# Performance work log

Hardware: AMD Instinct MI355X
Metric: run time of the kernel (lower is better)

Reference implementation:

```python
import jax, jax.numpy as jnp
import numpy as np

H = 64  # lstm hidden

def _lstm_scan(xs, h0, c0, wih, whh, bih, bhh):
    # xs: [T,B,D]; torch gate order i,f,g,o
    def step(carry, xt):
        h, c = carry
        gates = xt @ wih.T + h @ whh.T + bih + bhh
        i, f, g, o = jnp.split(gates, 4, axis=-1)
        c = jax.nn.sigmoid(f) * c + jax.nn.sigmoid(i) * jnp.tanh(g)
        h = jax.nn.sigmoid(o) * jnp.tanh(c)
        return (h, c), h
    (h, c), hs = jax.lax.scan(step, (h0, c0), xs)
    return hs, h, c


def setup_inputs() -> dict:
    key = jax.random.key(0)
    ks = jax.random.split(key, 32)
    r = lambda i, shape: (jax.random.normal(ks[i], shape, jnp.float32) * 0.05)
    B, T = 2048, 128
    inp = {
        "x": jax.random.normal(ks[0], (B, T, 37), jnp.float32),
        "enc_lin_w": r(1, (64, 37)), "enc_lin_b": r(2, (64,)),
        "enc_wih_f": r(3, (4 * H, 64)), "enc_whh_f": r(4, (4 * H, H)),
        "enc_bih_f": r(5, (4 * H,)), "enc_bhh_f": r(6, (4 * H,)),
        "enc_wih_b": r(7, (4 * H, 64)), "enc_whh_b": r(8, (4 * H, H)),
        "enc_bih_b": r(9, (4 * H,)), "enc_bhh_b": r(10, (4 * H,)),
        "att1_w": r(11, (32, 192)), "att1_b": r(12, (32,)),
        "att2_w": r(13, (1, 32)), "att2_b": r(14, (1,)),
        "dec_wih": r(15, (4 * H, 128)), "dec_whh": r(16, (4 * H, H)),
        "dec_bih": r(17, (4 * H,)), "dec_bhh": r(18, (4 * H,)),
        "dec_lin_w": r(19, (11, H)), "dec_lin_b": r(20, (11,)),
        "output_len": 10,
    }
    return inp


def reference(x, enc_lin_w, enc_lin_b,
              enc_wih_f, enc_whh_f, enc_bih_f, enc_bhh_f,
              enc_wih_b, enc_whh_b, enc_bih_b, enc_bhh_b,
              att1_w, att1_b, att2_w, att2_b,
              dec_wih, dec_whh, dec_bih, dec_bhh,
              dec_lin_w, dec_lin_b, output_len):
    B, T, _ = x.shape
    # ---- Encoder: linear -> relu -> BiLSTM ----
    e = jax.nn.relu(x @ enc_lin_w.T + enc_lin_b)          # [B,T,64]
    xs = jnp.transpose(e, (1, 0, 2))                       # [T,B,64]
    z = jnp.zeros((B, H), x.dtype)
    hf, _, _ = _lstm_scan(xs, z, z, enc_wih_f, enc_whh_f, enc_bih_f, enc_bhh_f)
    hb, _, _ = _lstm_scan(xs[::-1], z, z, enc_wih_b, enc_whh_b, enc_bih_b, enc_bhh_b)
    feats = jnp.concatenate([hf, hb[::-1]], axis=-1)       # [T,B,128]
    feats = jnp.transpose(feats, (1, 0, 2))                # [B,T,128]

    # ---- Decoder loop with (degenerate) additive attention ----
    def dec_step(carry, _):
        h, c = carry
        h_rep = jnp.broadcast_to(h[:, None, :], (B, T, H))
        fin = jnp.concatenate([feats, h_rep], axis=-1)     # [B,T,192]
        a = jnp.tanh(fin @ att1_w.T + att1_b)              # [B,T,32]
        s = a @ att2_w.T + att2_b                          # [B,T,1]
        scores = jax.nn.softmax(s, axis=-1)                # all ones (faithful to source)
        fd = jnp.sum(feats * scores, axis=1)               # [B,128]
        gates = fd @ dec_wih.T + h @ dec_whh.T + dec_bih + dec_bhh
        i, f, g, o = jnp.split(gates, 4, axis=-1)
        c = jax.nn.sigmoid(f) * c + jax.nn.sigmoid(i) * jnp.tanh(g)
        h = jax.nn.sigmoid(o) * jnp.tanh(c)
        out = jax.nn.softmax(h @ dec_lin_w.T + dec_lin_b, axis=-1)  # [B,11]
        return (h, c), out

    (_, _), outs = jax.lax.scan(dec_step, (z, z), None, length=output_len)
    return jnp.transpose(outs, (1, 0, 2))                  # [B,output_len,11]
```

## Files before the change

kernel.cpp:

```cpp
#include <hip/hip_runtime.h>


typedef _Float16 f16;
typedef f16 f16x8 __attribute__((ext_vector_type(8)));
typedef float f32x4 __attribute__((ext_vector_type(4)));

#define MFMA16(a, b, c) __builtin_amdgcn_mfma_f32_16x16x32_f16(a, b, c, 0, 0, 0)

__device__ __forceinline__ float sigf(float x) { return 1.f / (1.f + __expf(-x)); }
__device__ __forceinline__ float tanhf_fast(float x) {
  float e = __expf(2.f * x);
  return 1.f - 2.f / (e + 1.f);
}

#define NLOG2E  -1.4426950408889634f
#define N2LOG2E -2.8853900817779268f

__device__ __forceinline__ float rcp_(float x) { return __builtin_amdgcn_rcpf(x); }
__device__ __forceinline__ float ex2_(float x) { return __builtin_amdgcn_exp2f(x); }


__global__ __launch_bounds__(256) void enc_linear_k(
    const float* __restrict__ x, const float* __restrict__ w1,
    const float* __restrict__ b1, f16* __restrict__ efrag) {
  const int t = blockIdx.y;
  const int bblock = blockIdx.x;
  const int tid = threadIdx.x;
  const int w = tid >> 6, l = tid & 63;
  const int rho = l & 15, c = l >> 4;

  __shared__ float ldsw[64 * 37];
  __shared__ float ldsb[64];
  __shared__ __align__(16) f16 ldse[4][2][64][8];

  for (int i = tid; i < 64 * 37; i += 256) ldsw[i] = w1[i];
  if (tid < 64) ldsb[tid] = b1[tid];
  __syncthreads();

  f16x8 bw[4][2];
#pragma unroll
  for (int nt = 0; nt < 4; nt++) {
    const int kout = nt * 16 + rho;
#pragma unroll
    for (int ks = 0; ks < 2; ks++) {
      f16x8 v;
#pragma unroll
      for (int i = 0; i < 8; i++) {
        const int d = ks * 32 + c * 8 + i;
        v[i] = (f16)(d < 37 ? ldsw[kout * 37 + d] : 0.f);
      }
      bw[nt][ks] = v;
    }
  }

  const int brow = bblock * 64 + w * 16 + rho;
  const float* xrow = x + ((size_t)brow * 128 + t) * 37;
  f16x8 a0, a1;
#pragma unroll
  for (int i = 0; i < 8; i++) a0[i] = (f16)xrow[c * 8 + i];
#pragma unroll
  for (int i = 0; i < 8; i++) {
    const int d = 32 + c * 8 + i;
    a1[i] = (f16)((c == 0 && d < 37) ? xrow[d] : 0.f);
  }

  f32x4 acc[4] = {};
#pragma unroll
  for (int nt = 0; nt < 4; nt++) {
    acc[nt] = MFMA16(a0, bw[nt][0], acc[nt]);
    acc[nt] = MFMA16(a1, bw[nt][1], acc[nt]);
  }

#pragma unroll
  for (int nt = 0; nt < 4; nt++) {
    const int k = nt * 16 + rho;
#pragma unroll
    for (int r = 0; r < 4; r++) {
      const int bi = c * 4 + r;
      float v = acc[nt][r] + ldsb[k];
      v = fmaxf(v, 0.f);
      ldse[w][k >> 5][bi | (((k >> 3) & 3) << 4)][k & 7] = (f16)v;
    }
  }
  __syncthreads();
  const int bg = bblock * 4 + w;
  float4* dst = (float4*)efrag + ((size_t)(t * 128 + bg) * 2) * 64;
  const float4* src = (const float4*)&ldse[w][0][0][0];
  dst[l] = src[l];
  dst[64 + l] = src[64 + l];
}

__global__ __launch_bounds__(512, 2) void bilstm_k(
    const f16* __restrict__ efrag,
    const float* __restrict__ wih_f, const float* __restrict__ whh_f,
    const float* __restrict__ bih_f, const float* __restrict__ bhh_f,
    const float* __restrict__ wih_b, const float* __restrict__ whh_b,
    const float* __restrict__ bih_b, const float* __restrict__ bhh_b,
    float* __restrict__ fd) {
  const int bid = blockIdx.x;
  const int dir = bid >> 7;
  const int bg = bid & 127;
  const int tid = threadIdx.x;
  const int w = tid >> 6, l = tid & 63;
  const int rho = l & 15, c = l >> 4;
  const int gate = rho & 3, uoff = rho >> 2;

  const float* wih = dir ? wih_b : wih_f;
  const float* whh = dir ? whh_b : whh_f;
  const float* bih = dir ? bih_b : bih_f;
  const float* bhh = dir ? bhh_b : bhh_f;

  __shared__ __align__(16) f16 hbuf[2][2][64][8];
  {
    int* hz = (int*)hbuf;
    for (int i = tid; i < (int)(sizeof(hbuf) / 4); i += 512) hz[i] = 0;
  }

  const float sA = (gate == 2) ? N2LOG2E : NLOG2E;

  f16x8 aih[2][2], ahh[2][2];
#pragma unroll
  for (int q = 0; q < 2; q++) {
    const int m = 2 * w + q;
    const int n = gate * 64 + 4 * m + uoff;
#pragma unroll
    for (int ks = 0; ks < 2; ks++) {
      const float* p1 = wih + n * 64 + ks * 32 + c * 8;
      const float* p2 = whh + n * 64 + ks * 32 + c * 8;
      f16x8 v1, v2;
#pragma unroll
      for (int i = 0; i < 8; i++) {
        v1[i] = (f16)(p1[i] * sA);
        v2[i] = (f16)(p2[i] * sA);
      }
      aih[q][ks] = v1;
      ahh[q][ks] = v2;
    }
  }
  f32x4 bias[2];
#pragma unroll
  for (int q = 0; q < 2; q++) {
    const int j = 8 * w + 4 * q + c;
#pragma unroll
    for (int r = 0; r < 4; r++) {
      const float sr = (r == 2) ? N2LOG2E : NLOG2E;
      bias[q][r] = (bih[64 * r + j] + bhh[64 * r + j]) * sr;
    }
  }

  const f16x8* eb = (const f16x8*)efrag;
  const int tm0 = dir ? 127 : 0;
  const size_t idx0 = ((size_t)(tm0 * 128 + bg) * 2) * 64 + l;
  f16x8 ec0 = eb[idx0], ec1 = eb[idx0 + 64];
  f16x8 en0 = ec0, en1 = ec1;

  float cst[2] = {0.f, 0.f};
  float hs[2] = {0.f, 0.f};

  __syncthreads();

  for (int t = 0; t < 128; t++) {
    if (t + 1 < 128) {
      const int tm = dir ? 127 - (t + 1) : t + 1;
      const size_t idx = ((size_t)(tm * 128 + bg) * 2) * 64 + l;
      en0 = eb[idx];
      en1 = eb[idx + 64];
    }
    const int cur = t & 1;
    f16x8 h0 = *(const f16x8*)&hbuf[cur][0][l][0];
    f16x8 h1 = *(const f16x8*)&hbuf[cur][1][l][0];
#pragma unroll
    for (int q = 0; q < 2; q++) {
      f32x4 a = bias[q];
      a = MFMA16(aih[q][0], ec0, a);
      a = MFMA16(aih[q][1], ec1, a);
      a = MFMA16(ahh[q][0], h0, a);
      a = MFMA16(ahh[q][1], h1, a);
      const float ig = rcp_(1.f + ex2_(a[0]));
      const float fg = rcp_(1.f + ex2_(a[1]));
      const float gg = 2.f * rcp_(1.f + ex2_(a[2])) - 1.f;
      const float og = rcp_(1.f + ex2_(a[3]));
      cst[q] = fg * cst[q] + ig * gg;
      const float th = 2.f * rcp_(1.f + ex2_(cst[q] * N2LOG2E)) - 1.f;
      const float h = og * th;
      hs[q] += h;
      const int j = 8 * w + 4 * q + c;
      hbuf[cur ^ 1][j >> 5][rho | (((j >> 3) & 3) << 4)][j & 7] = (f16)h;
    }
    ec0 = en0;
    ec1 = en1;
    asm volatile("s_waitcnt lgkmcnt(0)\n\ts_barrier" ::: "memory");
  }
#pragma unroll
  for (int q = 0; q < 2; q++) {
    const int j = 8 * w + 4 * q + c;
    fd[(size_t)(bg * 16 + rho) * 128 + dir * 64 + j] = hs[q];
  }
}

__global__ __launch_bounds__(256) void decoder_k(
    const float* __restrict__ fd,
    const float* __restrict__ dwih, const float* __restrict__ dwhh,
    const float* __restrict__ dbih, const float* __restrict__ dbhh,
    const float* __restrict__ dlw, const float* __restrict__ dlb,
    const int* __restrict__ outlen_p, float* __restrict__ out) {
  const int b0 = blockIdx.x * 16;
  const int tid = threadIdx.x;
  const int w = tid >> 6, l = tid & 63;
  const int rho = l & 15, c = l >> 4;
  const int gate = rho & 3, uoff = rho >> 2;
  const int outlen = *outlen_p;

  __shared__ __align__(16) f16 hbuf[2][2][64][8];
  __shared__ float h32[64][16];
  __shared__ float ldslw[11 * 64];
  __shared__ float ldslb[16];
  __shared__ float lg[16][16];

  {
    int* hz = (int*)hbuf;
    for (int i = tid; i < (int)(sizeof(hbuf) / 4); i += 256) hz[i] = 0;
  }
  for (int i = tid; i < 704; i += 256) ldslw[i] = dlw[i];
  if (tid < 16) ldslb[tid] = (tid < 11) ? dlb[tid] : 0.f;

  f16x8 awhh[4][2];
  f32x4 acc0[4];
  {
    f16x8 bfd[4];
#pragma unroll
    for (int ks = 0; ks < 4; ks++) {
      const float* p = fd + (size_t)(b0 + rho) * 128 + ks * 32 + c * 8;
      f16x8 v;
#pragma unroll
      for (int i = 0; i < 8; i++) v[i] = (f16)p[i];
      bfd[ks] = v;
    }
#pragma unroll
    for (int q = 0; q < 4; q++) {
      const int m = 4 * w + q;
      const int n = gate * 64 + 4 * m + uoff;
      f32x4 a;
      const int j = 16 * w + 4 * q + c;
#pragma unroll
      for (int r = 0; r < 4; r++) a[r] = dbih[64 * r + j] + dbhh[64 * r + j];
#pragma unroll
      for (int ks = 0; ks < 4; ks++) {
        const float* p = dwih + n * 128 + ks * 32 + c * 8;
        f16x8 v;
#pragma unroll
        for (int i = 0; i < 8; i++) v[i] = (f16)p[i];
        a = MFMA16(v, bfd[ks], a);
      }
      acc0[q] = a;
#pragma unroll
      for (int ks = 0; ks < 2; ks++) {
        const float* p = dwhh + n * 64 + ks * 32 + c * 8;
        f16x8 v;
#pragma unroll
        for (int i = 0; i < 8; i++) v[i] = (f16)p[i];
        awhh[q][ks] = v;
      }
    }
  }
  float cst[4] = {0.f, 0.f, 0.f, 0.f};
  __syncthreads();

  for (int s = 0; s < outlen; s++) {
    const int cur = s & 1;
    f16x8 h0 = *(const f16x8*)&hbuf[cur][0][l][0];
    f16x8 h1 = *(const f16x8*)&hbuf[cur][1][l][0];
#pragma unroll
    for (int q = 0; q < 4; q++) {
      f32x4 a = acc0[q];
      a = MFMA16(awhh[q][0], h0, a);
      a = MFMA16(awhh[q][1], h1, a);
      const float ig = sigf(a[0]);
      const float fg = sigf(a[1]);
      const float gg = tanhf_fast(a[2]);
      const float og = sigf(a[3]);
      cst[q] = fg * cst[q] + ig * gg;
      const float h = og * tanhf_fast(cst[q]);
      const int j = 16 * w + 4 * q + c;
      hbuf[cur ^ 1][j >> 5][rho | (((j >> 3) & 3) << 4)][j & 7] = (f16)h;
      h32[j][rho] = h;
    }
    __syncthreads();
    const int b = tid >> 4, o = tid & 15;
    float logit = 0.f;
    if (o < 11) {
      logit = ldslb[o];
      for (int j = 0; j < 64; j++) logit += h32[j][b] * ldslw[o * 64 + j];
      lg[b][o] = logit;
    }
    __syncthreads();
    if (o < 11) {
      float mx = lg[b][0];
      for (int k = 1; k < 11; k++) mx = fmaxf(mx, lg[b][k]);
      float sum = 0.f;
      for (int k = 0; k < 11; k++) sum += __expf(lg[b][k] - mx);
      out[(size_t)(b0 + b) * outlen * 11 + (size_t)s * 11 + o] =
          __expf(logit - mx) / sum;
    }
    __syncthreads();
  }
}

extern "C" void kernel_launch(void* const* d_in, const int* in_sizes, int n_in,
                              void* d_out, int out_size, void* d_ws, size_t ws_size,
                              hipStream_t stream) {
  const float* x = (const float*)d_in[0];
  const float* w1 = (const float*)d_in[1];
  const float* b1 = (const float*)d_in[2];
  const float* wih_f = (const float*)d_in[3];
  const float* whh_f = (const float*)d_in[4];
  const float* bih_f = (const float*)d_in[5];
  const float* bhh_f = (const float*)d_in[6];
  const float* wih_b = (const float*)d_in[7];
  const float* whh_b = (const float*)d_in[8];
  const float* bih_b = (const float*)d_in[9];
  const float* bhh_b = (const float*)d_in[10];
  const float* dwih = (const float*)d_in[15];
  const float* dwhh = (const float*)d_in[16];
  const float* dbih = (const float*)d_in[17];
  const float* dbhh = (const float*)d_in[18];
  const float* dlw = (const float*)d_in[19];
  const float* dlb = (const float*)d_in[20];
  const int* outlen = (const int*)d_in[21];
  float* out = (float*)d_out;

  f16* efrag = (f16*)d_ws;
  float* fd = (float*)((char*)d_ws + (size_t)33554432);

  hipLaunchKernelGGL(enc_linear_k, dim3(32, 128), dim3(256), 0, stream,
                     x, w1, b1, efrag);
  hipLaunchKernelGGL(bilstm_k, dim3(256), dim3(512), 0, stream,
                     efrag, wih_f, whh_f, bih_f, bhh_f,
                     wih_b, whh_b, bih_b, bhh_b, fd);
  hipLaunchKernelGGL(decoder_k, dim3(128), dim3(256), 0, stream,
                     fd, dwih, dwhh, dbih, dbhh, dlw, dlb, outlen, out);
}
```

Baseline: 126.9 us.

## Fuse encoder linear into BiLSTM kernel and widen blocks to 16 waves

Removes the separate encoder-linear kernel and its fp16 intermediate buffer. Four of the BiLSTM block's waves now compute the next timestep's linear+relu from prefetched x rows and stage it into a double-buffered LDS tile. Blocks grow from 512 to 1024 threads, so each wave handles one gate tile instead of two, and the input and recurrent MFMA chains are split into two independent accumulators. This cuts global traffic and a launch, and shortens the per-step dependency chain, at the cost of extra per-step work on the encoder waves and more register pressure.

After: 154.7 us. 22.0% more time.

```diff
diff --git a/kernel.cpp b/kernel.cpp
--- a/kernel.cpp
+++ b/kernel.cpp
@@ -3,95 +3,26 @@
 
 typedef _Float16 f16;
 typedef f16 f16x8 __attribute__((ext_vector_type(8)));
+typedef f16 f16x4 __attribute__((ext_vector_type(4)));
 typedef float f32x4 __attribute__((ext_vector_type(4)));
 
 #define MFMA16(a, b, c) __builtin_amdgcn_mfma_f32_16x16x32_f16(a, b, c, 0, 0, 0)
 
+#define NLOG2E  -1.4426950408889634f
+#define N2LOG2E -2.8853900817779268f
+
+__device__ __forceinline__ float rcp_(float x) { return __builtin_amdgcn_rcpf(x); }
+__device__ __forceinline__ float ex2_(float x) { return __builtin_amdgcn_exp2f(x); }
 __device__ __forceinline__ float sigf(float x) { return 1.f / (1.f + __expf(-x)); }
 __device__ __forceinline__ float tanhf_fast(float x) {
   float e = __expf(2.f * x);
   return 1.f - 2.f / (e + 1.f);
 }
 
-#define NLOG2E  -1.4426950408889634f
-#define N2LOG2E -2.8853900817779268f
-
-__device__ __forceinline__ float rcp_(float x) { return __builtin_amdgcn_rcpf(x); }
-__device__ __forceinline__ float ex2_(float x) { return __builtin_amdgcn_exp2f(x); }
-
-
-__global__ __launch_bounds__(256) void enc_linear_k(
+
+__global__ __launch_bounds__(1024, 4) void bilstm_fused_k(
     const float* __restrict__ x, const float* __restrict__ w1,
-    const float* __restrict__ b1, f16* __restrict__ efrag) {
-  const int t = blockIdx.y;
-  const int bblock = blockIdx.x;
-  const int tid = threadIdx.x;
-  const int w = tid >> 6, l = tid & 63;
-  const int rho = l & 15, c = l >> 4;
-
-  __shared__ float ldsw[64 * 37];
-  __shared__ float ldsb[64];
-  __shared__ __align__(16) f16 ldse[4][2][64][8];
-
-  for (int i = tid; i < 64 * 37; i += 256) ldsw[i] = w1[i];
-  if (tid < 64) ldsb[tid] = b1[tid];
-  __syncthreads();
-
-  f16x8 bw[4][2];
-#pragma unroll
-  for (int nt = 0; nt < 4; nt++) {
-    const int kout = nt * 16 + rho;
-#pragma unroll
-    for (int ks = 0; ks < 2; ks++) {
-      f16x8 v;
-#pragma unroll
-      for (int i = 0; i < 8; i++) {
-        const int d = ks * 32 + c * 8 + i;
-        v[i] = (f16)(d < 37 ? ldsw[kout * 37 + d] : 0.f);
-      }
-      bw[nt][ks] = v;
-    }
-  }
-
-  const int brow = bblock * 64 + w * 16 + rho;
-  const float* xrow = x + ((size_t)brow * 128 + t) * 37;
-  f16x8 a0, a1;
-#pragma unroll
-  for (int i = 0; i < 8; i++) a0[i] = (f16)xrow[c * 8 + i];
-#pragma unroll
-  for (int i = 0; i < 8; i++) {
-    const int d = 32 + c * 8 + i;
-    a1[i] = (f16)((c == 0 && d < 37) ? xrow[d] : 0.f);
-  }
-
-  f32x4 acc[4] = {};
-#pragma unroll
-  for (int nt = 0; nt < 4; nt++) {
-    acc[nt] = MFMA16(a0, bw[nt][0], acc[nt]);
-    acc[nt] = MFMA16(a1, bw[nt][1], acc[nt]);
-  }
-
-#pragma unroll
-  for (int nt = 0; nt < 4; nt++) {
-    const int k = nt * 16 + rho;
-#pragma unroll
-    for (int r = 0; r < 4; r++) {
-      const int bi = c * 4 + r;
-      float v = acc[nt][r] + ldsb[k];
-      v = fmaxf(v, 0.f);
-      ldse[w][k >> 5][bi | (((k >> 3) & 3) << 4)][k & 7] = (f16)v;
-    }
-  }
-  __syncthreads();
-  const int bg = bblock * 4 + w;
-  float4* dst = (float4*)efrag + ((size_t)(t * 128 + bg) * 2) * 64;
-  const float4* src = (const float4*)&ldse[w][0][0][0];
-  dst[l] = src[l];
-  dst[64 + l] = src[64 + l];
-}
-
-__global__ __launch_bounds__(512, 2) void bilstm_k(
-    const f16* __restrict__ efrag,
+    const float* __restrict__ b1,
     const float* __restrict__ wih_f, const float* __restrict__ whh_f,
     const float* __restrict__ bih_f, const float* __restrict__ bhh_f,
     const float* __restrict__ wih_b, const float* __restrict__ whh_b,
@@ -111,91 +42,143 @@
   const float* bhh = dir ? bhh_b : bhh_f;
 
   __shared__ __align__(16) f16 hbuf[2][2][64][8];
-  {
-    int* hz = (int*)hbuf;
-    for (int i = tid; i < (int)(sizeof(hbuf) / 4); i += 512) hz[i] = 0;
-  }
+  __shared__ __align__(16) f16 ebuf[2][2][64][8];
+
+  { int* hz = (int*)hbuf; hz[tid] = 0; }
 
   const float sA = (gate == 2) ? N2LOG2E : NLOG2E;
-
-  f16x8 aih[2][2], ahh[2][2];
-#pragma unroll
-  for (int q = 0; q < 2; q++) {
-    const int m = 2 * w + q;
-    const int n = gate * 64 + 4 * m + uoff;
-#pragma unroll
-    for (int ks = 0; ks < 2; ks++) {
-      const float* p1 = wih + n * 64 + ks * 32 + c * 8;
-      const float* p2 = whh + n * 64 + ks * 32 + c * 8;
-      f16x8 v1, v2;
-#pragma unroll
-      for (int i = 0; i < 8; i++) {
-        v1[i] = (f16)(p1[i] * sA);
-        v2[i] = (f16)(p2[i] * sA);
-      }
-      aih[q][ks] = v1;
-      ahh[q][ks] = v2;
-    }
-  }
-  f32x4 bias[2];
-#pragma unroll
-  for (int q = 0; q < 2; q++) {
-    const int j = 8 * w + 4 * q + c;
-#pragma unroll
-    for (int r = 0; r < 4; r++) {
-      const float sr = (r == 2) ? N2LOG2E : NLOG2E;
-      bias[q][r] = (bih[64 * r + j] + bhh[64 * r + j]) * sr;
-    }
-  }
-
-  const f16x8* eb = (const f16x8*)efrag;
-  const int tm0 = dir ? 127 : 0;
-  const size_t idx0 = ((size_t)(tm0 * 128 + bg) * 2) * 64 + l;
-  f16x8 ec0 = eb[idx0], ec1 = eb[idx0 + 64];
-  f16x8 en0 = ec0, en1 = ec1;
-
-  float cst[2] = {0.f, 0.f};
-  float hs[2] = {0.f, 0.f};
+  const int n = gate * 64 + 4 * w + uoff;
+  f16x8 aih[2], ahh[2];
+#pragma unroll
+  for (int ks = 0; ks < 2; ks++) {
+    const float* p1 = wih + n * 64 + ks * 32 + c * 8;
+    const float* p2 = whh + n * 64 + ks * 32 + c * 8;
+    f16x8 v1, v2;
+#pragma unroll
+    for (int i = 0; i < 8; i++) {
+      v1[i] = (f16)(p1[i] * sA);
+      v2[i] = (f16)(p2[i] * sA);
+    }
+    aih[ks] = v1;
+    ahh[ks] = v2;
+  }
+  const int j = 4 * w + c;
+  f32x4 bias0;
+#pragma unroll
+  for (int r = 0; r < 4; r++) {
+    const float sr = (r == 2) ? N2LOG2E : NLOG2E;
+    bias0[r] = (bih[64 * r + j] + bhh[64 * r + j]) * sr;
+  }
+
+  const bool enc = (w < 4);
+  const int q = w;
+  f16x8 w1a0 = {}, w1a1 = {};
+  f32x4 eb = {};
+  float xc[8], xc2[5], xn[8], xn2[5];
+  const float* xrow = x + (size_t)(bg * 16 + rho) * 128 * 37;
+  if (enc) {
+#pragma unroll
+    for (int i = 0; i < 8; i++) w1a0[i] = (f16)w1[(16 * q + rho) * 37 + 8 * c + i];
+#pragma unroll
+    for (int i = 0; i < 8; i++) {
+      const int k = 32 + 8 * c + i;
+      w1a1[i] = (f16)((c == 0 && k < 37) ? w1[(16 * q + rho) * 37 + k] : 0.f);
+    }
+#pragma unroll
+    for (int r = 0; r < 4; r++) eb[r] = b1[16 * q + 4 * c + r];
+
+    {
+      const float* p = xrow + (dir ? 127 : 0) * 37;
+      float xt[8], xt2[5];
+#pragma unroll
+      for (int i = 0; i < 8; i++) xt[i] = p[8 * c + i];
+#pragma unroll
+      for (int i = 0; i < 5; i++) xt2[i] = (c == 0) ? p[32 + i] : 0.f;
+      f16x8 xb0, xb1;
+#pragma unroll
+      for (int i = 0; i < 8; i++) xb0[i] = (f16)xt[i];
+#pragma unroll
+      for (int i = 0; i < 8; i++) xb1[i] = (f16)(i < 5 ? xt2[i] : 0.f);
+      f32x4 ea = MFMA16(w1a0, xb0, eb);
+      ea = MFMA16(w1a1, xb1, ea);
+      f16x4 pk;
+#pragma unroll
+      for (int r = 0; r < 4; r++) pk[r] = (f16)fmaxf(ea[r], 0.f);
+      const int d0 = 16 * q + 4 * c;
+      *(f16x4*)&ebuf[0][q >> 1][rho | (((d0 >> 3) & 3) << 4)][d0 & 7] = pk;
+    }
+    {
+      const float* p = xrow + (dir ? 126 : 1) * 37;
+#pragma unroll
+      for (int i = 0; i < 8; i++) xc[i] = p[8 * c + i];
+#pragma unroll
+      for (int i = 0; i < 5; i++) xc2[i] = (c == 0) ? p[32 + i] : 0.f;
+    }
+    {
+      const float* p = xrow + (dir ? 125 : 2) * 37;
+#pragma unroll
+      for (int i = 0; i < 8; i++) xn[i] = p[8 * c + i];
+#pragma unroll
+      for (int i = 0; i < 5; i++) xn2[i] = (c == 0) ? p[32 + i] : 0.f;
+    }
+  }
+
+  float cst = 0.f, hs = 0.f;
+  const f32x4 z4 = {0.f, 0.f, 0.f, 0.f};
 
   __syncthreads();
 
   for (int t = 0; t < 128; t++) {
-    if (t + 1 < 128) {
-      const int tm = dir ? 127 - (t + 1) : t + 1;
-      const size_t idx = ((size_t)(tm * 128 + bg) * 2) * 64 + l;
-      en0 = eb[idx];
-      en1 = eb[idx + 64];
-    }
-    const int cur = t & 1;
+    const int cur = t & 1, nxt = cur ^ 1;
+    f16x8 e0 = *(const f16x8*)&ebuf[cur][0][l][0];
+    f16x8 e1 = *(const f16x8*)&ebuf[cur][1][l][0];
     f16x8 h0 = *(const f16x8*)&hbuf[cur][0][l][0];
     f16x8 h1 = *(const f16x8*)&hbuf[cur][1][l][0];
-#pragma unroll
-    for (int q = 0; q < 2; q++) {
-      f32x4 a = bias[q];
-      a = MFMA16(aih[q][0], ec0, a);
-      a = MFMA16(aih[q][1], ec1, a);
-      a = MFMA16(ahh[q][0], h0, a);
-      a = MFMA16(ahh[q][1], h1, a);
-      const float ig = rcp_(1.f + ex2_(a[0]));
-      const float fg = rcp_(1.f + ex2_(a[1]));
-      const float gg = 2.f * rcp_(1.f + ex2_(a[2])) - 1.f;
-      const float og = rcp_(1.f + ex2_(a[3]));
-      cst[q] = fg * cst[q] + ig * gg;
-      const float th = 2.f * rcp_(1.f + ex2_(cst[q] * N2LOG2E)) - 1.f;
-      const float h = og * th;
-      hs[q] += h;
-      const int j = 8 * w + 4 * q + c;
-      hbuf[cur ^ 1][j >> 5][rho | (((j >> 3) & 3) << 4)][j & 7] = (f16)h;
-    }
-    ec0 = en0;
-    ec1 = en1;
+    f32x4 a1 = MFMA16(aih[0], e0, bias0);
+    f32x4 a2 = MFMA16(aih[1], e1, z4);
+    a1 = MFMA16(ahh[0], h0, a1);
+    a2 = MFMA16(ahh[1], h1, a2);
+
+    if (enc && t + 1 < 128) {
+      f16x8 xb0, xb1;
+#pragma unroll
+      for (int i = 0; i < 8; i++) xb0[i] = (f16)xc[i];
+#pragma unroll
+      for (int i = 0; i < 8; i++) xb1[i] = (f16)(i < 5 ? xc2[i] : 0.f);
+      f32x4 ea = MFMA16(w1a0, xb0, eb);
+      ea = MFMA16(w1a1, xb1, ea);
+      f16x4 pk;
+#pragma unroll
+      for (int r = 0; r < 4; r++) pk[r] = (f16)fmaxf(ea[r], 0.f);
+      const int d0 = 16 * q + 4 * c;
+      *(f16x4*)&ebuf[nxt][q >> 1][rho | (((d0 >> 3) & 3) << 4)][d0 & 7] = pk;
+#pragma unroll
+      for (int i = 0; i < 8; i++) xc[i] = xn[i];
+#pragma unroll
+      for (int i = 0; i < 5; i++) xc2[i] = xn2[i];
+      const int s3 = (t + 3 < 128) ? t + 3 : 127;
+      const float* p = xrow + (dir ? 127 - s3 : s3) * 37;
+#pragma unroll
+      for (int i = 0; i < 8; i++) xn[i] = p[8 * c + i];
+#pragma unroll
+      for (int i = 0; i < 5; i++) xn2[i] = (c == 0) ? p[32 + i] : 0.f;
+    }
+
+    const f32x4 a = a1 + a2;
+    const float ig = rcp_(1.f + ex2_(a[0]));
+    const float fg = rcp_(1.f + ex2_(a[1]));
+    const float gg = 2.f * rcp_(1.f + ex2_(a[2])) - 1.f;
+    const float og = rcp_(1.f + ex2_(a[3]));
+    cst = fg * cst + ig * gg;
+    const float th = 2.f * rcp_(1.f + ex2_(cst * N2LOG2E)) - 1.f;
+    const float h = og * th;
+    hs += h;
+    hbuf[nxt][j >> 5][rho | (((j >> 3) & 3) << 4)][j & 7] = (f16)h;
+
     asm volatile("s_waitcnt lgkmcnt(0)\n\ts_barrier" ::: "memory");
   }
-#pragma unroll
-  for (int q = 0; q < 2; q++) {
-    const int j = 8 * w + 4 * q + c;
-    fd[(size_t)(bg * 16 + rho) * 128 + dir * 64 + j] = hs[q];
-  }
+
+  fd[(size_t)(bg * 16 + rho) * 128 + dir * 64 + j] = hs;
 }
 
 __global__ __launch_bounds__(256) void decoder_k(
@@ -290,7 +273,7 @@
     float logit = 0.f;
     if (o < 11) {
       logit = ldslb[o];
-      for (int j = 0; j < 64; j++) logit += h32[j][b] * ldslw[o * 64 + j];
+      for (int jj = 0; jj < 64; jj++) logit += h32[jj][b] * ldslw[o * 64 + jj];
       lg[b][o] = logit;
     }
     __syncthreads();
@@ -329,13 +312,10 @@
   const int* outlen = (const int*)d_in[21];
   float* out = (float*)d_out;
 
-  f16* efrag = (f16*)d_ws;
-  float* fd = (float*)((char*)d_ws + (size_t)33554432);
-
-  hipLaunchKernelGGL(enc_linear_k, dim3(32, 128), dim3(256), 0, stream,
-                     x, w1, b1, efrag);
-  hipLaunchKernelGGL(bilstm_k, dim3(256), dim3(512), 0, stream,
-                     efrag, wih_f, whh_f, bih_f, bhh_f,
+  float* fd = (float*)d_ws;
+
+  hipLaunchKernelGGL(bilstm_fused_k, dim3(256), dim3(1024), 0, stream,
+                     x, w1, b1, wih_f, whh_f, bih_f, bhh_f,
                      wih_b, whh_b, bih_b, bhh_b, fd);
   hipLaunchKernelGGL(decoder_k, dim3(128), dim3(256), 0, stream,
                      fd, dwih, dwhh, dbih, dbhh, dlw, dlb, outlen, out);
```

## Restructure encoder linear for coalesced x loads and deepen BiLSTM prefetch

Applied to the files above, without the earlier changes.

The encoder linear kernel now gives each block 16 batch rows and 8 consecutive timesteps. It stages the contiguous x slice in shared memory so global reads are coalesced, then computes with weights as the A operand and x as the B operand to produce the fragment layout directly. This replaces strided per-timestep row reads and the per-block weight re-fragmentation. In the BiLSTM loop the input-fragment prefetch goes from one step ahead to three, with a partially unrolled loop, to hide global load latency on the serial recurrence. The cost is more registers in a kernel bounded to two blocks per CU.

After: 136.6 us. 1.08x slower.

```diff
diff --git a/kernel.cpp b/kernel.cpp
--- a/kernel.cpp
+++ b/kernel.cpp
@@ -3,91 +3,83 @@
 
 typedef _Float16 f16;
 typedef f16 f16x8 __attribute__((ext_vector_type(8)));
+typedef f16 f16x4 __attribute__((ext_vector_type(4)));
 typedef float f32x4 __attribute__((ext_vector_type(4)));
 
 #define MFMA16(a, b, c) __builtin_amdgcn_mfma_f32_16x16x32_f16(a, b, c, 0, 0, 0)
 
+#define NLOG2E  -1.4426950408889634f
+#define N2LOG2E -2.8853900817779268f
+
+__device__ __forceinline__ float rcp_(float x) { return __builtin_amdgcn_rcpf(x); }
+__device__ __forceinline__ float ex2_(float x) { return __builtin_amdgcn_exp2f(x); }
 __device__ __forceinline__ float sigf(float x) { return 1.f / (1.f + __expf(-x)); }
 __device__ __forceinline__ float tanhf_fast(float x) {
   float e = __expf(2.f * x);
   return 1.f - 2.f / (e + 1.f);
 }
 
-#define NLOG2E  -1.4426950408889634f
-#define N2LOG2E -2.8853900817779268f
-
-__device__ __forceinline__ float rcp_(float x) { return __builtin_amdgcn_rcpf(x); }
-__device__ __forceinline__ float ex2_(float x) { return __builtin_amdgcn_exp2f(x); }
-
-
+
+#define TC 8
 __global__ __launch_bounds__(256) void enc_linear_k(
     const float* __restrict__ x, const float* __restrict__ w1,
     const float* __restrict__ b1, f16* __restrict__ efrag) {
-  const int t = blockIdx.y;
-  const int bblock = blockIdx.x;
+  const int bg = blockIdx.x;
+  const int tc = blockIdx.y;
   const int tid = threadIdx.x;
   const int w = tid >> 6, l = tid & 63;
   const int rho = l & 15, c = l >> 4;
 
+  __shared__ float xls[16][8 * 37 + 1];
   __shared__ float ldsw[64 * 37];
-  __shared__ float ldsb[64];
-  __shared__ __align__(16) f16 ldse[4][2][64][8];
+  __shared__ __align__(16) f16 fstage[TC][2][64][8];
 
   for (int i = tid; i < 64 * 37; i += 256) ldsw[i] = w1[i];
-  if (tid < 64) ldsb[tid] = b1[tid];
+#pragma unroll
+  for (int rr = 0; rr < 4; rr++) {
+    const int r = w * 4 + rr;
+    const float* src = x + ((size_t)(bg * 16 + r) * 128 + tc * TC) * 37;
+    for (int e = l; e < 296; e += 64) xls[r][e] = src[e];
+  }
   __syncthreads();
 
-  f16x8 bw[4][2];
-#pragma unroll
-  for (int nt = 0; nt < 4; nt++) {
-    const int kout = nt * 16 + rho;
-#pragma unroll
-    for (int ks = 0; ks < 2; ks++) {
-      f16x8 v;
-#pragma unroll
-      for (int i = 0; i < 8; i++) {
-        const int d = ks * 32 + c * 8 + i;
-        v[i] = (f16)(d < 37 ? ldsw[kout * 37 + d] : 0.f);
-      }
-      bw[nt][ks] = v;
-    }
-  }
-
-  const int brow = bblock * 64 + w * 16 + rho;
-  const float* xrow = x + ((size_t)brow * 128 + t) * 37;
   f16x8 a0, a1;
-#pragma unroll
-  for (int i = 0; i < 8; i++) a0[i] = (f16)xrow[c * 8 + i];
-#pragma unroll
-  for (int i = 0; i < 8; i++) {
-    const int d = 32 + c * 8 + i;
-    a1[i] = (f16)((c == 0 && d < 37) ? xrow[d] : 0.f);
-  }
-
-  f32x4 acc[4] = {};
-#pragma unroll
-  for (int nt = 0; nt < 4; nt++) {
-    acc[nt] = MFMA16(a0, bw[nt][0], acc[nt]);
-    acc[nt] = MFMA16(a1, bw[nt][1], acc[nt]);
-  }
-
-#pragma unroll
-  for (int nt = 0; nt < 4; nt++) {
-    const int k = nt * 16 + rho;
-#pragma unroll
-    for (int r = 0; r < 4; r++) {
-      const int bi = c * 4 + r;
-      float v = acc[nt][r] + ldsb[k];
-      v = fmaxf(v, 0.f);
-      ldse[w][k >> 5][bi | (((k >> 3) & 3) << 4)][k & 7] = (f16)v;
-    }
+  {
+    const float* pw = ldsw + (16 * w + rho) * 37;
+#pragma unroll
+    for (int i = 0; i < 8; i++) a0[i] = (f16)pw[8 * c + i];
+#pragma unroll
+    for (int i = 0; i < 8; i++) a1[i] = (f16)((c == 0 && i < 5) ? pw[32 + i] : 0.f);
+  }
+  f32x4 bias;
+#pragma unroll
+  for (int r = 0; r < 4; r++) bias[r] = b1[16 * w + 4 * c + r];
+
+#pragma unroll
+  for (int tl = 0; tl < TC; tl++) {
+    const float* px = &xls[rho][tl * 37];
+    f16x8 xb0, xb1;
+#pragma unroll
+    for (int i = 0; i < 8; i++) xb0[i] = (f16)px[8 * c + i];
+#pragma unroll
+    for (int i = 0; i < 8; i++) xb1[i] = (f16)((c == 0 && i < 5) ? px[32 + i] : 0.f);
+    f32x4 acc = bias;
+    acc = MFMA16(a0, xb0, acc);
+    acc = MFMA16(a1, xb1, acc);
+    f16x4 pk;
+#pragma unroll
+    for (int r = 0; r < 4; r++) pk[r] = (f16)fmaxf(acc[r], 0.f);
+    const int d0 = 16 * w + 4 * c;
+    *(f16x4*)&fstage[tl][w >> 1][rho | (((d0 >> 3) & 3) << 4)][d0 & 7] = pk;
   }
   __syncthreads();
-  const int bg = bblock * 4 + w;
-  float4* dst = (float4*)efrag + ((size_t)(t * 128 + bg) * 2) * 64;
-  const float4* src = (const float4*)&ldse[w][0][0][0];
-  dst[l] = src[l];
-  dst[64 + l] = src[64 + l];
+
+  const float4* srcf = (const float4*)fstage;
+  float4* dstf = (float4*)efrag;
+  for (int i = tid; i < TC * 2 * 64; i += 256) {
+    const int tl = i >> 7, rest = i & 127;
+    dstf[((size_t)((tc * TC + tl) * 128 + bg) * 2) * 64 + rest] = srcf[i];
+  }
 }
 
 __global__ __launch_bounds__(512, 2) void bilstm_k(
@@ -149,24 +141,23 @@
   }
 
   const f16x8* eb = (const f16x8*)efrag;
-  const int tm0 = dir ? 127 : 0;
-  const size_t idx0 = ((size_t)(tm0 * 128 + bg) * 2) * 64 + l;
-  f16x8 ec0 = eb[idx0], ec1 = eb[idx0 + 64];
-  f16x8 en0 = ec0, en1 = ec1;
+#define EIDX(t) (((size_t)(((dir ? 127 - (t) : (t)) * 128) + bg) * 2) * 64 + l)
+  f16x8 ec0 = eb[EIDX(0)], ec1 = eb[EIDX(0) + 64];
+  f16x8 e10 = eb[EIDX(1)], e11 = eb[EIDX(1) + 64];
+  f16x8 e20 = eb[EIDX(2)], e21 = eb[EIDX(2) + 64];
 
   float cst[2] = {0.f, 0.f};
   float hs[2] = {0.f, 0.f};
 
   __syncthreads();
 
+#pragma unroll 4
   for (int t = 0; t < 128; t++) {
-    if (t + 1 < 128) {
-      const int tm = dir ? 127 - (t + 1) : t + 1;
-      const size_t idx = ((size_t)(tm * 128 + bg) * 2) * 64 + l;
-      en0 = eb[idx];
-      en1 = eb[idx + 64];
-    }
     const int cur = t & 1;
+    const int t3 = (t + 3 < 128) ? t + 3 : 127;
+    const f16x8 ld0 = eb[EIDX(t3)];
+    const f16x8 ld1 = eb[EIDX(t3) + 64];
+
     f16x8 h0 = *(const f16x8*)&hbuf[cur][0][l][0];
     f16x8 h1 = *(const f16x8*)&hbuf[cur][1][l][0];
 #pragma unroll
@@ -187,10 +178,12 @@
       const int j = 8 * w + 4 * q + c;
       hbuf[cur ^ 1][j >> 5][rho | (((j >> 3) & 3) << 4)][j & 7] = (f16)h;
     }
-    ec0 = en0;
-    ec1 = en1;
+    ec0 = e10; ec1 = e11;
+    e10 = e20; e11 = e21;
+    e20 = ld0; e21 = ld1;
     asm volatile("s_waitcnt lgkmcnt(0)\n\ts_barrier" ::: "memory");
   }
+#undef EIDX
 #pragma unroll
   for (int q = 0; q < 2; q++) {
     const int j = 8 * w + 4 * q + c;
@@ -290,7 +283,7 @@
     float logit = 0.f;
     if (o < 11) {
       logit = ldslb[o];
-      for (int j = 0; j < 64; j++) logit += h32[j][b] * ldslw[o * 64 + j];
+      for (int jj = 0; jj < 64; jj++) logit += h32[jj][b] * ldslw[o * 64 + jj];
       lg[b][o] = logit;
     }
     __syncthreads();
@@ -332,7 +325,7 @@
   f16* efrag = (f16*)d_ws;
   float* fd = (float*)((char*)d_ws + (size_t)33554432);
 
-  hipLaunchKernelGGL(enc_linear_k, dim3(32, 128), dim3(256), 0, stream,
+  hipLaunchKernelGGL(enc_linear_k, dim3(128, 16), dim3(256), 0, stream,
                      x, w1, b1, efrag);
   hipLaunchKernelGGL(bilstm_k, dim3(256), dim3(512), 0, stream,
                      efrag, wih_f, whh_f, bih_f, bhh_f,
```
